# Optimization experiments

Hardware: AMD Instinct MI355X
Metric: run time of the kernel (lower is better)

Reference implementation:

```python
import jax, jax.numpy as jnp
import numpy as np


def setup_inputs() -> dict:
    key = jax.random.key(0)
    k1, k2 = jax.random.split(key)
    B, T, D, K = 16, 800, 256, 64
    x = jax.random.normal(k1, (B, T, D), dtype=jnp.float32)
    mu = jax.random.normal(k2, (K, D), dtype=jnp.float32)
    prec = jnp.ones((K,), dtype=jnp.float32)
    return {"x": x, "mu": mu, "prec": prec}


def reference(x, mu, prec):
    # x: (B,T,D), mu: (K,D), prec: (K,)
    delta = x[:, :, None, :] - mu[None, None, :, :]          # (B,T,K,D)
    dist = jnp.sum(delta * delta, axis=-1)                   # (B,T,K) dist_pow=2
    llk = -(prec * prec) * dist                              # use_bias=False -> bias=0
    r = jax.nn.softmax(llk, axis=-1)                         # softmax over components K
    r = r / (jnp.sum(r, axis=1, keepdims=True) + 1e-9)       # normalize over time T
    pool = jnp.einsum('btk,btkd->bkd', r, delta)             # weighted sum over T
    return pool.reshape(x.shape[0], -1)                      # (B, K*D)
```

## Files before the change

### kernel.cpp

```cpp
#include <hip/hip_runtime.h>

#define B_ 16
#define T_ 800
#define D_ 256
#define K_ 64
#define NTILE 13
#define TSPLIT 4

__global__ __launch_bounds__(256, 2) void kernelA(
    const float* __restrict__ x, const float* __restrict__ mu,
    const float* __restrict__ prec, float* __restrict__ r2, float* __restrict__ Spart)
{
    __shared__ float xs[64][68];
    __shared__ float mus[64][68];
    __shared__ float xxs[64];
    __shared__ float mms[64];
    __shared__ float sred[4][64];

    const int tid  = threadIdx.x;
    const int tx   = tid >> 4;
    const int ky   = tid & 15;
    const int b    = blockIdx.x / NTILE;
    const int tile = blockIdx.x % NTILE;
    const int t0   = tile * 64;

    float acc[4][4];
    #pragma unroll
    for (int i = 0; i < 4; ++i)
        #pragma unroll
        for (int j = 0; j < 4; ++j) acc[i][j] = 0.f;

    const int srow = tid >> 2, sq = tid & 3;
    float xxp = 0.f, mmp = 0.f;

    #pragma unroll 1
    for (int c = 0; c < 4; ++c) {
        __syncthreads();
        #pragma unroll
        for (int q = 0; q < 4; ++q) {
            const int row  = q * 16 + tx;
            int trow = t0 + row; if (trow > T_ - 1) trow = T_ - 1;
            *(float4*)&xs[row][ky * 4] =
                *(const float4*)(x + (size_t)(b * T_ + trow) * D_ + c * 64 + ky * 4);
            *(float4*)&mus[row][ky * 4] =
                *(const float4*)(mu + (size_t)row * D_ + c * 64 + ky * 4);
        }
        __syncthreads();
        #pragma unroll
        for (int m = 0; m < 4; ++m) {
            float4 v = *(const float4*)&xs[srow][sq * 16 + m * 4];
            xxp = fmaf(v.x, v.x, xxp); xxp = fmaf(v.y, v.y, xxp);
            xxp = fmaf(v.z, v.z, xxp); xxp = fmaf(v.w, v.w, xxp);
            float4 u = *(const float4*)&mus[srow][sq * 16 + m * 4];
            mmp = fmaf(u.x, u.x, mmp); mmp = fmaf(u.y, u.y, mmp);
            mmp = fmaf(u.z, u.z, mmp); mmp = fmaf(u.w, u.w, mmp);
        }
        #pragma unroll 4
        for (int dg = 0; dg < 16; ++dg) {
            float4 xv[4], mv[4];
            #pragma unroll
            for (int i = 0; i < 4; ++i) xv[i] = *(const float4*)&xs[tx * 4 + i][dg * 4];
            #pragma unroll
            for (int j = 0; j < 4; ++j) mv[j] = *(const float4*)&mus[ky + 16 * j][dg * 4];
            #pragma unroll
            for (int i = 0; i < 4; ++i)
                #pragma unroll
                for (int j = 0; j < 4; ++j) {
                    float a = acc[i][j];
                    a = fmaf(xv[i].x, mv[j].x, a);
                    a = fmaf(xv[i].y, mv[j].y, a);
                    a = fmaf(xv[i].z, mv[j].z, a);
                    a = fmaf(xv[i].w, mv[j].w, a);
                    acc[i][j] = a;
                }
        }
    }

    xxp += __shfl_xor(xxp, 1); xxp += __shfl_xor(xxp, 2);
    mmp += __shfl_xor(mmp, 1); mmp += __shfl_xor(mmp, 2);
    if (sq == 0) { xxs[srow] = xxp; mms[srow] = mmp; }
    __syncthreads();

    float p2[4], mmk[4];
    #pragma unroll
    for (int j = 0; j < 4; ++j) {
        float p = prec[ky + 16 * j];
        p2[j] = p * p;
        mmk[j] = mms[ky + 16 * j];
    }

    float sacc[4] = {0.f, 0.f, 0.f, 0.f};
    #pragma unroll
    for (int i = 0; i < 4; ++i) {
        const int tl = tx * 4 + i;
        const bool valid = (t0 + tl) < T_;
        const float xxv = xxs[tl];
        float llk[4];
        #pragma unroll
        for (int j = 0; j < 4; ++j)
            llk[j] = p2[j] * (2.f * acc[i][j] - xxv - mmk[j]);
        float mx = fmaxf(fmaxf(llk[0], llk[1]), fmaxf(llk[2], llk[3]));
        mx = fmaxf(mx, __shfl_xor(mx, 1)); mx = fmaxf(mx, __shfl_xor(mx, 2));
        mx = fmaxf(mx, __shfl_xor(mx, 4)); mx = fmaxf(mx, __shfl_xor(mx, 8));
        float e[4], ps = 0.f;
        #pragma unroll
        for (int j = 0; j < 4; ++j) { e[j] = __expf(llk[j] - mx); ps += e[j]; }
        ps += __shfl_xor(ps, 1); ps += __shfl_xor(ps, 2);
        ps += __shfl_xor(ps, 4); ps += __shfl_xor(ps, 8);
        const float inv = 1.f / ps;
        float4 rv;
        rv.x = e[0] * inv; rv.y = e[1] * inv; rv.z = e[2] * inv; rv.w = e[3] * inv;
        if (valid) {
            *(float4*)(r2 + (size_t)(b * T_ + t0 + tl) * K_ + ky * 4) = rv;
            sacc[0] += rv.x; sacc[1] += rv.y; sacc[2] += rv.z; sacc[3] += rv.w;
        }
    }
    #pragma unroll
    for (int j = 0; j < 4; ++j) {
        sacc[j] += __shfl_xor(sacc[j], 16);
        sacc[j] += __shfl_xor(sacc[j], 32);
    }
    const int w = tid >> 6;
    if ((tid & 48) == 0) {
        #pragma unroll
        for (int j = 0; j < 4; ++j) sred[w][ky * 4 + j] = sacc[j];
    }
    __syncthreads();
    if (tid < 64) {
        const int k = tid;
        const int slot = (k & 15) * 4 + (k >> 4);
        float s = sred[0][slot] + sred[1][slot] + sred[2][slot] + sred[3][slot];
        Spart[((size_t)b * NTILE + tile) * K_ + k] = s;
    }
}

__global__ __launch_bounds__(256, 2) void kernelB(
    const float* __restrict__ x, const float* __restrict__ r2, float* __restrict__ Pp)
{
    __shared__ float xs[25][68];
    __shared__ float rs[25][68];

    const int tid = threadIdx.x;
    const int kx  = tid >> 4;
    const int dy  = tid & 15;
    const int bid = blockIdx.x;
    const int b   = bid >> 4;
    const int dc  = (bid >> 2) & 3;
    const int ts  = bid & 3;

    float4 acc[4];
    #pragma unroll
    for (int j = 0; j < 4; ++j) acc[j] = make_float4(0.f, 0.f, 0.f, 0.f);

    #pragma unroll 1
    for (int sc = 0; sc < 8; ++sc) {
        const int tbase = ts * 200 + sc * 25;
        __syncthreads();
        #pragma unroll
        for (int jj = 0; jj < 2; ++jj) {
            const int idx = tid + jj * 256;
            if (idx < 400) {
                const int row = idx >> 4, f4i = idx & 15;
                *(float4*)&xs[row][f4i * 4] =
                    *(const float4*)(x + (size_t)(b * T_ + tbase + row) * D_ + dc * 64 + f4i * 4);
                *(float4*)&rs[row][f4i * 4] =
                    *(const float4*)(r2 + (size_t)(b * T_ + tbase + row) * K_ + f4i * 4);
            }
        }
        __syncthreads();
        #pragma unroll 5
        for (int tt = 0; tt < 25; ++tt) {
            const float4 rv = *(const float4*)&rs[tt][kx * 4];
            const float4 xv = *(const float4*)&xs[tt][dy * 4];
            acc[0].x = fmaf(rv.x, xv.x, acc[0].x); acc[0].y = fmaf(rv.x, xv.y, acc[0].y);
            acc[0].z = fmaf(rv.x, xv.z, acc[0].z); acc[0].w = fmaf(rv.x, xv.w, acc[0].w);
            acc[1].x = fmaf(rv.y, xv.x, acc[1].x); acc[1].y = fmaf(rv.y, xv.y, acc[1].y);
            acc[1].z = fmaf(rv.y, xv.z, acc[1].z); acc[1].w = fmaf(rv.y, xv.w, acc[1].w);
            acc[2].x = fmaf(rv.z, xv.x, acc[2].x); acc[2].y = fmaf(rv.z, xv.y, acc[2].y);
            acc[2].z = fmaf(rv.z, xv.z, acc[2].z); acc[2].w = fmaf(rv.z, xv.w, acc[2].w);
            acc[3].x = fmaf(rv.w, xv.x, acc[3].x); acc[3].y = fmaf(rv.w, xv.y, acc[3].y);
            acc[3].z = fmaf(rv.w, xv.z, acc[3].z); acc[3].w = fmaf(rv.w, xv.w, acc[3].w);
        }
    }

    #pragma unroll
    for (int j = 0; j < 4; ++j) {
        const int k = kx + 16 * j;
        *(float4*)(Pp + (((size_t)ts * B_ + b) * K_ + k) * D_ + dc * 64 + dy * 4) = acc[j];
    }
}

__global__ __launch_bounds__(64) void kernelC(
    const float* __restrict__ Pp, const float* __restrict__ Spart,
    const float* __restrict__ mu, float* __restrict__ out)
{
    const int bk   = blockIdx.x;
    const int b    = bk >> 6, k = bk & 63;
    const int lane = threadIdx.x;

    float s = 0.f;
    #pragma unroll
    for (int p = 0; p < NTILE; ++p)
        s += Spart[((size_t)b * NTILE + p) * K_ + k];

    float4 acc = make_float4(0.f, 0.f, 0.f, 0.f);
    #pragma unroll
    for (int ts = 0; ts < TSPLIT; ++ts) {
        float4 v = ((const float4*)(Pp + (((size_t)ts * B_ + b) * K_ + k) * D_))[lane];
        acc.x += v.x; acc.y += v.y; acc.z += v.z; acc.w += v.w;
    }
    const float inv = 1.f / (s + 1e-9f);
    const float sm  = s * inv;
    float4 m = ((const float4*)(mu + (size_t)k * D_))[lane];
    float4 o;
    o.x = acc.x * inv - sm * m.x;
    o.y = acc.y * inv - sm * m.y;
    o.z = acc.z * inv - sm * m.z;
    o.w = acc.w * inv - sm * m.w;
    ((float4*)out)[(size_t)bk * 64 + lane] = o;
}

extern "C" void kernel_launch(void* const* d_in, const int* in_sizes, int n_in,
                              void* d_out, int out_size, void* d_ws, size_t ws_size,
                              hipStream_t stream) {
    const float* x    = (const float*)d_in[0];
    const float* mu   = (const float*)d_in[1];
    const float* prec = (const float*)d_in[2];
    float* out = (float*)d_out;

    float* r2    = (float*)d_ws;
    float* Pp    = r2 + (size_t)B_ * T_ * K_;
    float* Spart = Pp + (size_t)TSPLIT * B_ * K_ * D_;

    kernelA<<<B_ * NTILE, 256, 0, stream>>>(x, mu, prec, r2, Spart);
    kernelB<<<B_ * 4 * TSPLIT, 256, 0, stream>>>(x, r2, Pp);
    kernelC<<<B_ * K_, 64, 0, stream>>>(Pp, Spart, mu, out);
}
```

Measured before the change: 97.85 us.

## Widen kernelA to 512 threads with full-D smem, double kernelB T-split, flatten kernelC

kernelA now loads the whole 64x256 x and mu tiles into shared memory in one pass and uses 512 threads, each computing a 2x4 tile of the dot products, so the per-chunk synchronisation loop goes away and more threads are in flight per block. kernelB splits T into 8 parts instead of 4, doubling the grid and processing 50-row chunks, to give more blocks on the GPU. kernelC is reorganised into 256 blocks of 256 threads over flat float4 outputs. The cost is about 130KB of LDS per kernelA block, which limits it to one block per CU, plus twice as many partial-sum buffers for kernelC to read and reduce.

```diff
diff --git a/kernel.cpp b/kernel.cpp
--- a/kernel.cpp
+++ b/kernel.cpp
@@ -5,17 +5,17 @@
 #define D_ 256
 #define K_ 64
 #define NTILE 13
-#define TSPLIT 4
-
-__global__ __launch_bounds__(256, 2) void kernelA(
+#define TSPLIT 8
+
+__global__ __launch_bounds__(512, 1) void kernelA(
     const float* __restrict__ x, const float* __restrict__ mu,
     const float* __restrict__ prec, float* __restrict__ r2, float* __restrict__ Spart)
 {
-    __shared__ float xs[64][68];
-    __shared__ float mus[64][68];
+    __shared__ float xs[64 * 260];
+    __shared__ float mus[64 * 260];
     __shared__ float xxs[64];
     __shared__ float mms[64];
-    __shared__ float sred[4][64];
+    __shared__ float sred[8][64];
 
     const int tid  = threadIdx.x;
     const int tx   = tid >> 4;
@@ -24,62 +24,61 @@
     const int tile = blockIdx.x % NTILE;
     const int t0   = tile * 64;
 
-    float acc[4][4];
-    #pragma unroll
-    for (int i = 0; i < 4; ++i)
-        #pragma unroll
-        for (int j = 0; j < 4; ++j) acc[i][j] = 0.f;
-
-    const int srow = tid >> 2, sq = tid & 3;
-    float xxp = 0.f, mmp = 0.f;
-
-    #pragma unroll 1
-    for (int c = 0; c < 4; ++c) {
-        __syncthreads();
-        #pragma unroll
-        for (int q = 0; q < 4; ++q) {
-            const int row  = q * 16 + tx;
-            int trow = t0 + row; if (trow > T_ - 1) trow = T_ - 1;
-            *(float4*)&xs[row][ky * 4] =
-                *(const float4*)(x + (size_t)(b * T_ + trow) * D_ + c * 64 + ky * 4);
-            *(float4*)&mus[row][ky * 4] =
-                *(const float4*)(mu + (size_t)row * D_ + c * 64 + ky * 4);
-        }
-        __syncthreads();
-        #pragma unroll
-        for (int m = 0; m < 4; ++m) {
-            float4 v = *(const float4*)&xs[srow][sq * 16 + m * 4];
+    #pragma unroll
+    for (int jj = 0; jj < 8; ++jj) {
+        const int g   = tid + jj * 512;
+        const int row = g >> 6, col = g & 63;
+        int trow = t0 + row; if (trow > T_ - 1) trow = T_ - 1;
+        *(float4*)&xs[row * 260 + col * 4] =
+            *(const float4*)(x + ((size_t)(b * T_ + trow)) * D_ + col * 4);
+        *(float4*)&mus[row * 260 + col * 4] =
+            *(const float4*)(mu + (size_t)row * D_ + col * 4);
+    }
+    __syncthreads();
+
+    {
+        const int srow = tid >> 3, sq = tid & 7;
+        float xxp = 0.f, mmp = 0.f;
+        #pragma unroll
+        for (int m = 0; m < 8; ++m) {
+            float4 v = *(const float4*)&xs[srow * 260 + (sq * 8 + m) * 4];
             xxp = fmaf(v.x, v.x, xxp); xxp = fmaf(v.y, v.y, xxp);
             xxp = fmaf(v.z, v.z, xxp); xxp = fmaf(v.w, v.w, xxp);
-            float4 u = *(const float4*)&mus[srow][sq * 16 + m * 4];
+            float4 u = *(const float4*)&mus[srow * 260 + (sq * 8 + m) * 4];
             mmp = fmaf(u.x, u.x, mmp); mmp = fmaf(u.y, u.y, mmp);
             mmp = fmaf(u.z, u.z, mmp); mmp = fmaf(u.w, u.w, mmp);
         }
-        #pragma unroll 4
-        for (int dg = 0; dg < 16; ++dg) {
-            float4 xv[4], mv[4];
+        xxp += __shfl_xor(xxp, 1); xxp += __shfl_xor(xxp, 2); xxp += __shfl_xor(xxp, 4);
+        mmp += __shfl_xor(mmp, 1); mmp += __shfl_xor(mmp, 2); mmp += __shfl_xor(mmp, 4);
+        if (sq == 0) { xxs[srow] = xxp; mms[srow] = mmp; }
+    }
+    __syncthreads();
+
+    float acc[2][4];
+    #pragma unroll
+    for (int i = 0; i < 2; ++i)
+        #pragma unroll
+        for (int j = 0; j < 4; ++j) acc[i][j] = 0.f;
+
+    #pragma unroll 4
+    for (int dg = 0; dg < 64; ++dg) {
+        float4 xv[2], mv[4];
+        #pragma unroll
+        for (int i = 0; i < 2; ++i) xv[i] = *(const float4*)&xs[(tx * 2 + i) * 260 + dg * 4];
+        #pragma unroll
+        for (int j = 0; j < 4; ++j) mv[j] = *(const float4*)&mus[(ky + 16 * j) * 260 + dg * 4];
+        #pragma unroll
+        for (int i = 0; i < 2; ++i)
             #pragma unroll
-            for (int i = 0; i < 4; ++i) xv[i] = *(const float4*)&xs[tx * 4 + i][dg * 4];
-            #pragma unroll
-            for (int j = 0; j < 4; ++j) mv[j] = *(const float4*)&mus[ky + 16 * j][dg * 4];
-            #pragma unroll
-            for (int i = 0; i < 4; ++i)
-                #pragma unroll
-                for (int j = 0; j < 4; ++j) {
-                    float a = acc[i][j];
-                    a = fmaf(xv[i].x, mv[j].x, a);
-                    a = fmaf(xv[i].y, mv[j].y, a);
-                    a = fmaf(xv[i].z, mv[j].z, a);
-                    a = fmaf(xv[i].w, mv[j].w, a);
-                    acc[i][j] = a;
-                }
-        }
-    }
-
-    xxp += __shfl_xor(xxp, 1); xxp += __shfl_xor(xxp, 2);
-    mmp += __shfl_xor(mmp, 1); mmp += __shfl_xor(mmp, 2);
-    if (sq == 0) { xxs[srow] = xxp; mms[srow] = mmp; }
-    __syncthreads();
+            for (int j = 0; j < 4; ++j) {
+                float a = acc[i][j];
+                a = fmaf(xv[i].x, mv[j].x, a);
+                a = fmaf(xv[i].y, mv[j].y, a);
+                a = fmaf(xv[i].z, mv[j].z, a);
+                a = fmaf(xv[i].w, mv[j].w, a);
+                acc[i][j] = a;
+            }
+    }
 
     float p2[4], mmk[4];
     #pragma unroll
@@ -91,8 +90,8 @@
 
     float sacc[4] = {0.f, 0.f, 0.f, 0.f};
     #pragma unroll
-    for (int i = 0; i < 4; ++i) {
-        const int tl = tx * 4 + i;
+    for (int i = 0; i < 2; ++i) {
+        const int tl = tx * 2 + i;
         const bool valid = (t0 + tl) < T_;
         const float xxv = xxs[tl];
         float llk[4];
@@ -115,6 +114,7 @@
             sacc[0] += rv.x; sacc[1] += rv.y; sacc[2] += rv.z; sacc[3] += rv.w;
         }
     }
+
     #pragma unroll
     for (int j = 0; j < 4; ++j) {
         sacc[j] += __shfl_xor(sacc[j], 16);
@@ -129,7 +129,9 @@
     if (tid < 64) {
         const int k = tid;
         const int slot = (k & 15) * 4 + (k >> 4);
-        float s = sred[0][slot] + sred[1][slot] + sred[2][slot] + sred[3][slot];
+        float s = 0.f;
+        #pragma unroll
+        for (int q = 0; q < 8; ++q) s += sred[q][slot];
         Spart[((size_t)b * NTILE + tile) * K_ + k] = s;
     }
 }
@@ -137,41 +139,41 @@
 __global__ __launch_bounds__(256, 2) void kernelB(
     const float* __restrict__ x, const float* __restrict__ r2, float* __restrict__ Pp)
 {
-    __shared__ float xs[25][68];
-    __shared__ float rs[25][68];
+    __shared__ float xs[50 * 68];
+    __shared__ float rs[50 * 68];
 
     const int tid = threadIdx.x;
     const int kx  = tid >> 4;
     const int dy  = tid & 15;
     const int bid = blockIdx.x;
-    const int b   = bid >> 4;
-    const int dc  = (bid >> 2) & 3;
-    const int ts  = bid & 3;
+    const int b   = bid >> 5;
+    const int dc  = (bid >> 3) & 3;
+    const int ts  = bid & 7;
 
     float4 acc[4];
     #pragma unroll
     for (int j = 0; j < 4; ++j) acc[j] = make_float4(0.f, 0.f, 0.f, 0.f);
 
     #pragma unroll 1
-    for (int sc = 0; sc < 8; ++sc) {
-        const int tbase = ts * 200 + sc * 25;
+    for (int sc = 0; sc < 2; ++sc) {
+        const int tbase = ts * 100 + sc * 50;
         __syncthreads();
         #pragma unroll
-        for (int jj = 0; jj < 2; ++jj) {
+        for (int jj = 0; jj < 4; ++jj) {
             const int idx = tid + jj * 256;
-            if (idx < 400) {
+            if (idx < 800) {
                 const int row = idx >> 4, f4i = idx & 15;
-                *(float4*)&xs[row][f4i * 4] =
+                *(float4*)&xs[row * 68 + f4i * 4] =
                     *(const float4*)(x + (size_t)(b * T_ + tbase + row) * D_ + dc * 64 + f4i * 4);
-                *(float4*)&rs[row][f4i * 4] =
+                *(float4*)&rs[row * 68 + f4i * 4] =
                     *(const float4*)(r2 + (size_t)(b * T_ + tbase + row) * K_ + f4i * 4);
             }
         }
         __syncthreads();
         #pragma unroll 5
-        for (int tt = 0; tt < 25; ++tt) {
-            const float4 rv = *(const float4*)&rs[tt][kx * 4];
-            const float4 xv = *(const float4*)&xs[tt][dy * 4];
+        for (int tt = 0; tt < 50; ++tt) {
+            const float4 rv = *(const float4*)&rs[tt * 68 + kx * 4];
+            const float4 xv = *(const float4*)&xs[tt * 68 + dy * 4];
             acc[0].x = fmaf(rv.x, xv.x, acc[0].x); acc[0].y = fmaf(rv.x, xv.y, acc[0].y);
             acc[0].z = fmaf(rv.x, xv.z, acc[0].z); acc[0].w = fmaf(rv.x, xv.w, acc[0].w);
             acc[1].x = fmaf(rv.y, xv.x, acc[1].x); acc[1].y = fmaf(rv.y, xv.y, acc[1].y);
@@ -190,13 +192,14 @@
     }
 }
 
-__global__ __launch_bounds__(64) void kernelC(
+__global__ __launch_bounds__(256) void kernelC(
     const float* __restrict__ Pp, const float* __restrict__ Spart,
     const float* __restrict__ mu, float* __restrict__ out)
 {
-    const int bk   = blockIdx.x;
-    const int b    = bk >> 6, k = bk & 63;
-    const int lane = threadIdx.x;
+    const int o4 = blockIdx.x * 256 + threadIdx.x;
+    const int d4 = o4 & 63;
+    const int k  = (o4 >> 6) & 63;
+    const int b  = o4 >> 12;
 
     float s = 0.f;
     #pragma unroll
@@ -206,18 +209,18 @@
     float4 acc = make_float4(0.f, 0.f, 0.f, 0.f);
     #pragma unroll
     for (int ts = 0; ts < TSPLIT; ++ts) {
-        float4 v = ((const float4*)(Pp + (((size_t)ts * B_ + b) * K_ + k) * D_))[lane];
+        float4 v = ((const float4*)Pp)[(((size_t)ts * B_ + b) * K_ + k) * 64 + d4];
         acc.x += v.x; acc.y += v.y; acc.z += v.z; acc.w += v.w;
     }
     const float inv = 1.f / (s + 1e-9f);
     const float sm  = s * inv;
-    float4 m = ((const float4*)(mu + (size_t)k * D_))[lane];
+    float4 m = ((const float4*)mu)[k * 64 + d4];
     float4 o;
     o.x = acc.x * inv - sm * m.x;
     o.y = acc.y * inv - sm * m.y;
     o.z = acc.z * inv - sm * m.z;
     o.w = acc.w * inv - sm * m.w;
-    ((float4*)out)[(size_t)bk * 64 + lane] = o;
+    ((float4*)out)[o4] = o;
 }
 
 extern "C" void kernel_launch(void* const* d_in, const int* in_sizes, int n_in,
@@ -232,7 +235,7 @@
     float* Pp    = r2 + (size_t)B_ * T_ * K_;
     float* Spart = Pp + (size_t)TSPLIT * B_ * K_ * D_;
 
-    kernelA<<<B_ * NTILE, 256, 0, stream>>>(x, mu, prec, r2, Spart);
+    kernelA<<<B_ * NTILE, 512, 0, stream>>>(x, mu, prec, r2, Spart);
     kernelB<<<B_ * 4 * TSPLIT, 256, 0, stream>>>(x, r2, Pp);
-    kernelC<<<B_ * K_, 64, 0, stream>>>(Pp, Spart, mu, out);
-}
+    kernelC<<<256, 256, 0, stream>>>(Pp, Spart, mu, out);
+}
```

Measured after the change: 88.93 us. 9.1% less time.
